# Performance work log

Measured on AMD Instinct MI355X. Metric: run time of the kernel, lower is better.

## Reference

```python
import jax, jax.numpy as jnp
import numpy as np

H = 64   # hid_dim (hard-coded in Attn_LSTM)
C = 8    # enc_in / out_dim
L = 96   # enc_seq_len = interval*lag = max_length
T = 24   # pre_len = window*horizon
B = 4096


def _p(key, shape, scale=0.1):
    return (jax.random.normal(key, shape, dtype=jnp.float32) * scale)


def setup_inputs() -> dict:
    key = jax.random.key(0)
    ks = jax.random.split(key, 20)
    inp = {
        'x_enc': jax.random.normal(ks[0], (B, L, C), dtype=jnp.float32),
        'x_mark_enc': jax.random.normal(ks[1], (B, L, 4), dtype=jnp.float32),
        'x_dec': jax.random.normal(ks[2], (B, T, C), dtype=jnp.float32),
        'x_mark_dec': jax.random.normal(ks[3], (B, T, 4), dtype=jnp.float32),
        # encoder LSTM (1 layer, input C -> hid H), pytorch gate order i,f,g,o
        'enc_Wih': _p(ks[4], (4 * H, C)), 'enc_Whh': _p(ks[5], (4 * H, H)),
        'enc_bih': _p(ks[6], (4 * H,)), 'enc_bhh': _p(ks[7], (4 * H,)),
        # decoder
        'emb_W': _p(ks[8], (H, C)), 'emb_b': _p(ks[9], (H,)),
        'attn_W': _p(ks[10], (L, 2 * H)), 'attn_b': _p(ks[11], (L,)),
        'comb_W': _p(ks[12], (H, 2 * H)), 'comb_b': _p(ks[13], (H,)),
        'dec_Wih': _p(ks[14], (4 * H, H)), 'dec_Whh': _p(ks[15], (4 * H, H)),
        'dec_bih': _p(ks[16], (4 * H,)), 'dec_bhh': _p(ks[17], (4 * H,)),
        'out_W': _p(ks[18], (C, H)), 'out_b': _p(ks[19], (C,)),
    }
    return inp


def _lstm_cell(x, h, c, Wih, Whh, bih, bhh):
    g = x @ Wih.T + h @ Whh.T + (bih + bhh)
    i, f, gg, o = jnp.split(g, 4, axis=-1)
    i, f, o = jax.nn.sigmoid(i), jax.nn.sigmoid(f), jax.nn.sigmoid(o)
    c_new = f * c + i * jnp.tanh(gg)
    h_new = o * jnp.tanh(c_new)
    return h_new, c_new


def _forward(x_enc, enc_Wih, enc_Whh, enc_bih, enc_bhh,
             emb_W, emb_b, attn_W, attn_b, comb_W, comb_b,
             dec_Wih, dec_Whh, dec_bih, dec_bhh, out_W, out_b):
    seq_last = x_enc[:, -1:, :]               # [B,1,C]
    x = x_enc - seq_last                      # normalized

    # ---- encoder: 1-layer LSTM over L steps ----
    h0 = jnp.zeros((x.shape[0], H), dtype=x.dtype)
    c0 = jnp.zeros_like(h0)

    def enc_step(carry, xt):
        h, c = carry
        h, c = _lstm_cell(xt, h, c, enc_Wih, enc_Whh, enc_bih, enc_bhh)
        return (h, c), h

    (h_enc, c_enc), enc_out = jax.lax.scan(enc_step, (h0, c0),
                                           jnp.swapaxes(x, 0, 1))
    enc_out = jnp.swapaxes(enc_out, 0, 1)     # [B,L,H]

    # ---- attention decoder: T sequential steps ----
    dec_in0 = x[:, -1, :]                     # last (normalized) input, [B,C]

    def dec_step(carry, _):
        inp, h, c = carry
        emb = jax.nn.relu(inp @ emb_W.T + emb_b)                       # [B,H]
        aw = jax.nn.softmax(jnp.concatenate([emb, h], -1) @ attn_W.T + attn_b)  # [B,L]
        ctx = jnp.einsum('bl,blh->bh', aw, enc_out)                    # [B,H]
        comb = jnp.concatenate([emb, ctx], -1) @ comb_W.T + comb_b     # [B,H]
        h, c = _lstm_cell(comb, h, c, dec_Wih, dec_Whh, dec_bih, dec_bhh)
        pred = h @ out_W.T + out_b                                     # [B,C]
        # original code feeds prediction.detach() back in
        return (jax.lax.stop_gradient(pred), h, c), (pred, aw)

    _, (preds, aws) = jax.lax.scan(dec_step, (dec_in0, h_enc, c_enc),
                                   None, length=T)
    pre_y = jnp.swapaxes(preds, 0, 1) + seq_last   # [B,T,C]
    return pre_y


def reference(x_enc, x_mark_enc, x_dec, x_mark_dec,
              enc_Wih, enc_Whh, enc_bih, enc_bhh,
              emb_W, emb_b, attn_W, attn_b, comb_W, comb_b,
              dec_Wih, dec_Whh, dec_bih, dec_bhh, out_W, out_b):
    # x_mark_enc, x_dec, x_mark_dec are accepted but unused (as in original)
    return _forward(x_enc, enc_Wih, enc_Whh, enc_bih, enc_bhh,
                    emb_W, emb_b, attn_W, attn_b, comb_W, comb_b,
                    dec_Wih, dec_Whh, dec_bih, dec_bhh, out_W, out_b)
```

## Files before the change

### kernel.cpp

```cpp
#include <hip/hip_runtime.h>

#define LL 96
#define TT 24
#define HH 64
#define CC 8
#define GG 256
#define BT 8
#define NB 512

typedef unsigned short u16t;
typedef unsigned int   u32t;
typedef __attribute__((ext_vector_type(8))) short bf16x8;
typedef __attribute__((ext_vector_type(4))) float f32x4;

__device__ __forceinline__ float b2f(u16t u){ union{u32t i; float f;} v; v.i=((u32t)u)<<16; return v.f; }
__device__ __forceinline__ float lo2f(u32t p){ union{u32t i; float f;} v; v.i=p<<16; return v.f; }
__device__ __forceinline__ float hi2f(u32t p){ union{u32t i; float f;} v; v.i=p&0xffff0000u; return v.f; }
__device__ __forceinline__ u16t f2b(float f){ union{float f; u32t i;} v; v.f=f; u32t l=(v.i>>16)&1u; v.i+=0x7fffu+l; return (u16t)(v.i>>16); }
__device__ __forceinline__ float rcpf(float x){ return __builtin_amdgcn_rcpf(x); }
__device__ __forceinline__ float sigm(float x){ return rcpf(1.f + __expf(-x)); }
__device__ __forceinline__ float tanh2(float x){ return 1.f - 2.f*rcpf(__expf(2.f*x) + 1.f); }
__device__ __forceinline__ u32t pk2(float a, float b){ return (u32t)f2b(a) | ((u32t)f2b(b)<<16); }
__device__ __forceinline__ bf16x8 u2b8(uint4 u){ union{uint4 a; bf16x8 b;} v; v.a=u; return v.b; }
__device__ __forceinline__ int aaddr(int k, int m){ return (((k>>5)*4 + ((k>>3)&3))*16 + m)*8 + (k&7); }

template<bool F32> __device__ __forceinline__ float ldf(const void* p, size_t i){
    if constexpr (F32) return ((const float*)p)[i];
    else               return b2f(((const u16t*)p)[i]);
}
template<bool F32> __device__ __forceinline__ uint4 ld8p(const void* p, size_t i){
    if constexpr (F32){
        const float* f = (const float*)p + i;
        uint4 r; r.x = pk2(f[0],f[1]); r.y = pk2(f[2],f[3]);
                 r.z = pk2(f[4],f[5]); r.w = pk2(f[6],f[7]);
        return r;
    } else return *(const uint4*)((const u16t*)p + i);
}
template<bool F32> __device__ __forceinline__ void stf(void* p, size_t i, float v){
    if constexpr (F32) ((float*)p)[i] = v;
    else               ((u16t*)p)[i] = f2b(v);
}
template<bool F32> __device__ __forceinline__ float ldW_enc(const void* wih, const void* whh, int r, int k){
    if (k < CC)      return ldf<F32>(wih, (size_t)r*CC + k);
    else if (k < 72) return ldf<F32>(whh, (size_t)r*HH + (k-CC));
    else             return 0.f;
}

__device__ __forceinline__ bool inputs_are_f32(const void* bih){
    const u16t* p = (const u16t*)bih;
    int cnt = 0;
    #pragma unroll
    for (int i = 0; i < 64; ++i){
        u32t e = ((u32t)p[i] >> 7) & 0xFFu;
        cnt += (e >= 128u) ? 1 : 0;
    }
    return cnt > 0;
}

template<bool F32>
__global__ __launch_bounds__(256,2) void fused_g(
    const void* __restrict__ x_enc,
    const void* __restrict__ eWih, const void* __restrict__ eWhh,
    const void* __restrict__ ebih, const void* __restrict__ ebhh,
    const void* __restrict__ embW, const void* __restrict__ embb,
    const void* __restrict__ attnW, const void* __restrict__ attnb,
    const void* __restrict__ combW, const void* __restrict__ combb,
    const void* __restrict__ dWih, const void* __restrict__ dWhh,
    const void* __restrict__ dbih, const void* __restrict__ dbhh,
    const void* __restrict__ outW, const void* __restrict__ outb,
    void* __restrict__ outp, u16t* __restrict__ eoG)
{
    if (inputs_are_f32(ebih) != F32) return;

    __shared__ __align__(16) float slp[CC*10];
    __shared__ __align__(16) short Abuf2[2][1536];
    __shared__ __align__(16) char  uni[18880];

    const int tid = threadIdx.x;
    const int b0  = blockIdx.x * BT;
    const int col = tid & 15, quad = (tid >> 4) & 3, wv = tid >> 6;
    const int r0  = (quad >> 1) * 2;

    bf16x8 Bf[4][3];
    float  biasg[4];
    #pragma unroll
    for (int g = 0; g < 4; ++g){
        int r = g*64 + wv*16 + col;
        biasg[g] = ldf<F32>(ebih, r) + ldf<F32>(ebhh, r);
        #pragma unroll
        for (int kb = 0; kb < 3; ++kb){
            bf16x8 v;
            #pragma unroll
            for (int x = 0; x < 8; ++x){
                int k = kb*32 + quad*8 + x;
                v[x] = (short)f2b(ldW_enc<F32>(eWih, eWhh, r, k));
            }
            Bf[g][kb] = v;
        }
    }
    for (int n = tid; n < 2*1536; n += 256) ((short*)Abuf2)[n] = 0;
    float sl = 0.f; size_t xbase = 0;
    if (tid < BT*CC){ int b = tid >> 3, i = tid & 7;
        xbase = (size_t)(b0+b)*(LL*CC) + i;
        sl = ldf<F32>(x_enc, xbase + (size_t)(LL-1)*CC);
        slp[i*10 + b] = sl; }
    __syncthreads();
    if (tid < BT*CC){ short v = (short)f2b(ldf<F32>(x_enc, xbase) - sl);
        Abuf2[0][tid] = v; Abuf2[0][tid + 64] = v; }
    float xr = (tid < BT*CC) ? ldf<F32>(x_enc, xbase + CC) : 0.f;

    const int jmy = wv*16 + col;
    const int kh  = 8 + jmy;
    const int hwbase = aaddr(kh, 0);

    u32t ebase[2];
    #pragma unroll
    for (int rr = 0; rr < 2; ++rr){
        u32t bg = (u32t)(b0 + ((quad*4 + r0 + rr) & 7));
        ebase[rr] = (bg*4u + (u32t)(jmy>>4))*1536u + (u32t)((jmy&15)*8);
    }

    float creg[2] = {0.f,0.f};
    u16t  hb16[2] = {0,0};

    for (int t = 0; t < LL; ++t){
        __syncthreads();
        const bf16x8* AbR = (const bf16x8*)Abuf2[t & 1];
        short*        AbW = Abuf2[(t + 1) & 1];
        bf16x8 a0 = AbR[(0*4 + quad)*16 + col];
        bf16x8 a1 = AbR[(1*4 + quad)*16 + col];
        bf16x8 a2 = AbR[(2*4 + quad)*16 + col];
        f32x4 acc[4];
        #pragma unroll
        for (int g = 0; g < 4; ++g){
            f32x4 a; a[0]=biasg[g]; a[1]=biasg[g]; a[2]=biasg[g]; a[3]=biasg[g];
            a = __builtin_amdgcn_mfma_f32_16x16x32_bf16(a0, Bf[g][0], a, 0,0,0);
            a = __builtin_amdgcn_mfma_f32_16x16x32_bf16(a1, Bf[g][1], a, 0,0,0);
            a = __builtin_amdgcn_mfma_f32_16x16x32_bf16(a2, Bf[g][2], a, 0,0,0);
            acc[g] = a;
        }
        int off = (t>>5)*512 + ((t>>3)&3)*128 + (t&7);
        #pragma unroll
        for (int rr = 0; rr < 2; ++rr){
            int r = r0 + rr;
            int b = (quad*4 + r) & 7;
            float c = sigm(acc[1][r])*creg[rr] + sigm(acc[0][r])*tanh2(acc[2][r]);
            float h = sigm(acc[3][r])*tanh2(c);
            creg[rr] = c; hb16[rr] = f2b(h);
            eoG[ebase[rr] + off] = hb16[rr];
            AbW[hwbase + b*8]     = (short)hb16[rr];
            AbW[hwbase + (b+8)*8] = (short)hb16[rr];
        }
        if (tid < BT*CC && t < LL-1){
            short v = (short)f2b(xr - sl);
            AbW[tid] = v; AbW[tid + 64] = v;
            int tn = (t+2 < LL) ? t+2 : LL-1;
            xr = ldf<F32>(x_enc, xbase + (size_t)tn*CC);
        }
    }

    bf16x8 Bd[4][4];
    #pragma unroll
    for (int g = 0; g < 4; ++g){
        int r = g*64 + wv*16 + col;
        Bd[g][0] = u2b8(ld8p<F32>(dWih, (size_t)r*HH + quad*8));
        Bd[g][1] = u2b8(ld8p<F32>(dWih, (size_t)r*HH + 32 + quad*8));
        Bd[g][2] = u2b8(ld8p<F32>(dWhh, (size_t)r*HH + quad*8));
        Bd[g][3] = u2b8(ld8p<F32>(dWhh, (size_t)r*HH + 32 + quad*8));
    }
    bf16x8 Ba[2][4];
    #pragma unroll
    for (int kb = 0; kb < 4; ++kb)
        Ba[0][kb] = u2b8(ld8p<F32>(attnW, (size_t)(wv*16+col)*128 + kb*32 + quad*8));
    if (wv < 2){
        #pragma unroll
        for (int kb = 0; kb < 4; ++kb)
            Ba[1][kb] = u2b8(ld8p<F32>(attnW, (size_t)((4+wv)*16+col)*128 + kb*32 + quad*8));
    } else {
        #pragma unroll
        for (int kb = 0; kb < 4; ++kb) Ba[1][kb] = Ba[0][kb];
    }
    bf16x8 Bc[4];
    #pragma unroll
    for (int kb = 0; kb < 4; ++kb)
        Bc[kb] = u2b8(ld8p<F32>(combW, (size_t)(wv*16+col)*128 + kb*32 + quad*8));
    bf16x8 zz = {0,0,0,0,0,0,0,0};
    bf16x8 eBf = zz;
    if (quad == 0) eBf = u2b8(ld8p<F32>(embW, (size_t)(wv*16+col)*CC));
    bf16x8 oBf0 = zz, oBf1 = zz;
    if (col < CC){
        oBf0 = u2b8(ld8p<F32>(outW, (size_t)col*HH + quad*8));
        oBf1 = u2b8(ld8p<F32>(outW, (size_t)col*HH + 32 + quad*8));
    }

    float* decB  = (float*)(uni + 0);
    float* attnB = (float*)(uni + 1024);
    float* embB  = (float*)(uni + 1408);
    float* combB = (float*)(uni + 1664);
    float* outB  = (float*)(uni + 1920);
    float* Lg    = (float*)(uni + 1952);
    u16t*  awB   = (u16t*)(uni + 5024);
    u16t*  Ae    = (u16t*)(uni + 6560);
    u16t*  Ah0   = (u16t*)(uni + 8608);
    u16t*  Ah1   = (u16t*)(uni + 10656);
    u16t*  Actx  = (u16t*)(uni + 12704);
    u16t*  Acmb  = (u16t*)(uni + 14752);
    u16t*  Apred = (u16t*)(uni + 16800);

    #pragma unroll
    for (int rr = 0; rr < 2; ++rr){
        int b = (quad*4 + r0 + rr) & 7;
        Ah0[aaddr(jmy, b)]     = hb16[rr];
        Ah0[aaddr(jmy, b+8)]   = hb16[rr];
    }
    decB[tid] = ldf<F32>(dbih, tid) + ldf<F32>(dbhh, tid);
    if (tid < LL) attnB[tid] = ldf<F32>(attnb, tid);
    if (tid < HH) embB[tid]  = ldf<F32>(embb, tid);
    if (tid < HH) combB[tid] = ldf<F32>(combb, tid);
    if (tid < CC) outB[tid]  = ldf<F32>(outb, tid);
    for (int n = tid; n < 1024; n += 256) Apred[n] = 0;
    __syncthreads();

    const u16t* ebp = eoG + (size_t)(b0 + wv*2) * 6144;
    uint4 eF0[12], eF1[12];
    #pragma unroll
    for (int f = 0; f < 12; ++f) eF0[f] = *(const uint4*)(ebp + f*512 + quad*128 + col*8);
    #pragma unroll
    for (int f = 0; f < 12; ++f) eF1[f] = *(const uint4*)(ebp + 6144 + f*512 + quad*128 + col*8);

    const int lgS = tid & 31, bS = tid >> 5;
    const bf16x8* AeV   = (const bf16x8*)Ae;
    const bf16x8* ActxV = (const bf16x8*)Actx;
    const bf16x8* AcmbV = (const bf16x8*)Acmb;
    const bf16x8* ApV   = (const bf16x8*)Apred;

    for (int t = 0; t < TT; ++t){
        u16t* AhR = (t & 1) ? Ah1 : Ah0;
        u16t* AhW = (t & 1) ? Ah0 : Ah1;
        const bf16x8* AhV = (const bf16x8*)AhR;

        {
            bf16x8 ap = ApV[quad*16 + col];
            float eb = embB[wv*16 + col];
            f32x4 a; a[0]=eb; a[1]=eb; a[2]=eb; a[3]=eb;
            a = __builtin_amdgcn_mfma_f32_16x16x32_bf16(ap, eBf, a, 0,0,0);
            #pragma unroll
            for (int r = 0; r < 4; ++r)
                Ae[aaddr(wv*16+col, quad*4 + r)] = f2b(fmaxf(a[r], 0.f));
        }
        __syncthreads();

        {
            bf16x8 ae0 = AeV[(0*4+quad)*16 + col], ae1 = AeV[(1*4+quad)*16 + col];
            bf16x8 ah0 = AhV[(0*4+quad)*16 + col], ah1 = AhV[(1*4+quad)*16 + col];
            const int ns = (wv < 2) ? 2 : 1;
            for (int s = 0; s < ns; ++s){
                int lt = (s == 0) ? wv : 4+wv;
                float bz = attnB[lt*16 + col];
                f32x4 a; a[0]=bz; a[1]=bz; a[2]=bz; a[3]=bz;
                a = __builtin_amdgcn_mfma_f32_16x16x32_bf16(ae0, Ba[s][0], a, 0,0,0);
                a = __builtin_amdgcn_mfma_f32_16x16x32_bf16(ae1, Ba[s][1], a, 0,0,0);
                a = __builtin_amdgcn_mfma_f32_16x16x32_bf16(ah0, Ba[s][2], a, 0,0,0);
                a = __builtin_amdgcn_mfma_f32_16x16x32_bf16(ah1, Ba[s][3], a, 0,0,0);
                if (quad < 2)
                    *(float4*)&Lg[(lt*16+col)*8 + quad*4] = make_float4(a[0],a[1],a[2],a[3]);
            }
        }
        __syncthreads();

        {
            int l = lgS*3;
            float ev0 = Lg[l*8 + bS], ev1 = Lg[(l+1)*8 + bS], ev2 = Lg[(l+2)*8 + bS];
            float mx = fmaxf(ev0, fmaxf(ev1, ev2));
            #pragma unroll
            for (int m = 16; m >= 1; m >>= 1) mx = fmaxf(mx, __shfl_xor(mx, m, 32));
            float e0 = __expf(ev0 - mx), e1 = __expf(ev1 - mx), e2 = __expf(ev2 - mx);
            float sm = e0 + e1 + e2;
            #pragma unroll
            for (int m = 16; m >= 1; m >>= 1) sm += __shfl_xor(sm, m, 32);
            float inv = rcpf(sm);
            awB[bS*96 + l]     = f2b(e0*inv);
            awB[bS*96 + l + 1] = f2b(e1*inv);
            awB[bS*96 + l + 2] = f2b(e2*inv);
        }
        {
            const u16t* ap0 = awB + (wv*2)*96;
            bf16x8 f0 = *(const bf16x8*)(ap0 + quad*8);
            bf16x8 f1 = *(const bf16x8*)(ap0 + 32 + quad*8);
            bf16x8 f2 = *(const bf16x8*)(ap0 + 64 + quad*8);
            #pragma unroll
            for (int nt = 0; nt < 4; ++nt){
                f32x4 a; a[0]=0.f; a[1]=0.f; a[2]=0.f; a[3]=0.f;
                a = __builtin_amdgcn_mfma_f32_16x16x32_bf16(f0, u2b8(eF0[nt*3+0]), a, 0,0,0);
                a = __builtin_amdgcn_mfma_f32_16x16x32_bf16(f1, u2b8(eF0[nt*3+1]), a, 0,0,0);
                a = __builtin_amdgcn_mfma_f32_16x16x32_bf16(f2, u2b8(eF0[nt*3+2]), a, 0,0,0);
                if (quad == 0){
                    u16t v = f2b(a[0]);
                    Actx[aaddr(nt*16+col, wv*2)]   = v;
                    Actx[aaddr(nt*16+col, wv*2+8)] = v;
                }
            }
            const u16t* ap1 = awB + (wv*2+1)*96;
            bf16x8 g0 = *(const bf16x8*)(ap1 + quad*8);
            bf16x8 g1 = *(const bf16x8*)(ap1 + 32 + quad*8);
            bf16x8 g2 = *(const bf16x8*)(ap1 + 64 + quad*8);
            #pragma unroll
            for (int nt = 0; nt < 4; ++nt){
                f32x4 a; a[0]=0.f; a[1]=0.f; a[2]=0.f; a[3]=0.f;
                a = __builtin_amdgcn_mfma_f32_16x16x32_bf16(g0, u2b8(eF1[nt*3+0]), a, 0,0,0);
                a = __builtin_amdgcn_mfma_f32_16x16x32_bf16(g1, u2b8(eF1[nt*3+1]), a, 0,0,0);
                a = __builtin_amdgcn_mfma_f32_16x16x32_bf16(g2, u2b8(eF1[nt*3+2]), a, 0,0,0);
                if (quad == 0){
                    u16t v = f2b(a[0]);
                    Actx[aaddr(nt*16+col, wv*2+1)] = v;
                    Actx[aaddr(nt*16+col, wv*2+9)] = v;
                }
            }
        }
        __syncthreads();

        {
            bf16x8 ae0 = AeV[(0*4+quad)*16 + col],   ae1 = AeV[(1*4+quad)*16 + col];
            bf16x8 ax0 = ActxV[(0*4+quad)*16 + col], ax1 = ActxV[(1*4+quad)*16 + col];
            float bz = combB[wv*16 + col];
            f32x4 a; a[0]=bz; a[1]=bz; a[2]=bz; a[3]=bz;
            a = __builtin_amdgcn_mfma_f32_16x16x32_bf16(ae0, Bc[0], a, 0,0,0);
            a = __builtin_amdgcn_mfma_f32_16x16x32_bf16(ae1, Bc[1], a, 0,0,0);
            a = __builtin_amdgcn_mfma_f32_16x16x32_bf16(ax0, Bc[2], a, 0,0,0);
            a = __builtin_amdgcn_mfma_f32_16x16x32_bf16(ax1, Bc[3], a, 0,0,0);
            #pragma unroll
            for (int r = 0; r < 4; ++r)
                Acmb[aaddr(wv*16+col, quad*4 + r)] = f2b(a[r]);
        }
        __syncthreads();

        {
            bf16x8 ac0 = AcmbV[(0*4+quad)*16 + col], ac1 = AcmbV[(1*4+quad)*16 + col];
            bf16x8 ah0 = AhV[(0*4+quad)*16 + col],   ah1 = AhV[(1*4+quad)*16 + col];
            f32x4 g4[4];
            #pragma unroll
            for (int g = 0; g < 4; ++g){
                float bz = decB[g*64 + wv*16 + col];
                f32x4 a; a[0]=bz; a[1]=bz; a[2]=bz; a[3]=bz;
                a = __builtin_amdgcn_mfma_f32_16x16x32_bf16(ac0, Bd[g][0], a, 0,0,0);
                a = __builtin_amdgcn_mfma_f32_16x16x32_bf16(ac1, Bd[g][1], a, 0,0,0);
                a = __builtin_amdgcn_mfma_f32_16x16x32_bf16(ah0, Bd[g][2], a, 0,0,0);
                a = __builtin_amdgcn_mfma_f32_16x16x32_bf16(ah1, Bd[g][3], a, 0,0,0);
                g4[g] = a;
            }
            #pragma unroll
            for (int rr = 0; rr < 2; ++rr){
                int r = r0 + rr;
                int b = (quad*4 + r) & 7;
                float c = sigm(g4[1][r])*creg[rr] + sigm(g4[0][r])*tanh2(g4[2][r]);
                float h = sigm(g4[3][r])*tanh2(c);
                creg[rr] = c;
                u16t hv = f2b(h);
                AhW[aaddr(jmy, b)]   = hv;
                AhW[aaddr(jmy, b+8)] = hv;
            }
        }
        __syncthreads();

        if (wv == 0){
            const bf16x8* AhWV = (const bf16x8*)AhW;
            bf16x8 xh0 = AhWV[(0*4+quad)*16 + col];
            bf16x8 xh1 = AhWV[(1*4+quad)*16 + col];
            float ob = outB[col & 7];
            f32x4 a; a[0]=ob; a[1]=ob; a[2]=ob; a[3]=ob;
            a = __builtin_amdgcn_mfma_f32_16x16x32_bf16(xh0, oBf0, a, 0,0,0);
            a = __builtin_amdgcn_mfma_f32_16x16x32_bf16(xh1, oBf1, a, 0,0,0);
            if (col < CC){
                #pragma unroll
                for (int r = 0; r < 4; ++r){
                    int m = quad*4 + r, b = m & 7;
                    float p = a[r];
                    Apred[aaddr(col, m)] = f2b(p);
                    if (m < 8)
                        stf<F32>(outp, ((size_t)(b0+b)*TT + t)*CC + col, p + slp[col*10 + b]);
                }
            }
        }
        __syncthreads();
    }
}

extern "C" void kernel_launch(void* const* d_in, const int* in_sizes, int n_in,
                              void* d_out, int out_size, void* d_ws, size_t ws_size,
                              hipStream_t stream)
{
    (void)in_sizes; (void)n_in; (void)out_size; (void)ws_size;
    fused_g<false><<<NB, 256, 0, stream>>>(
        d_in[0],
        d_in[4],  d_in[5],  d_in[6],  d_in[7],
        d_in[8],  d_in[9],  d_in[10], d_in[11],
        d_in[12], d_in[13], d_in[14], d_in[15],
        d_in[16], d_in[17], d_in[18], d_in[19],
        d_out, (u16t*)d_ws);
    fused_g<true><<<NB, 256, 0, stream>>>(
        d_in[0],
        d_in[4],  d_in[5],  d_in[6],  d_in[7],
        d_in[8],  d_in[9],  d_in[10], d_in[11],
        d_in[12], d_in[13], d_in[14], d_in[15],
        d_in[16], d_in[17], d_in[18], d_in[19],
        d_out, (u16t*)d_ws);
}
```

Measured before the change: 293.4 us.

## Split fused kernel into 4-row encoder kernel and separate decoder kernel

Splits the fused LSTM kernel in two. The encoder runs 4 batch rows per block on 1024 blocks with 4 blocks per CU, so each lane computes one hidden unit instead of two, and it stores packed bf16 pairs of encoder outputs. The final cell state goes to a workspace buffer, and a separate decoder kernel with 8 rows per block reads the final h and c back. This is meant to raise occupancy and shorten the serial encoder critical path. The cost is extra launches and a global round trip of state, and the new path only runs when the workspace is large enough; otherwise the old fused path is used.

```diff
diff --git a/kernel.cpp b/kernel.cpp
--- a/kernel.cpp
+++ b/kernel.cpp
@@ -58,106 +58,120 @@
 }
 
 template<bool F32>
-__global__ __launch_bounds__(256,2) void fused_g(
+__global__ __launch_bounds__(256,4) void enc4_g(
     const void* __restrict__ x_enc,
     const void* __restrict__ eWih, const void* __restrict__ eWhh,
     const void* __restrict__ ebih, const void* __restrict__ ebhh,
+    u16t* __restrict__ eoG, float* __restrict__ cG)
+{
+    if (inputs_are_f32(ebih) != F32) return;
+
+    __shared__ __align__(16) short Abuf2[2][1536];
+
+    const int tid = threadIdx.x;
+    const int b0  = blockIdx.x * 4;
+    const int col = tid & 15, quad = (tid >> 4) & 3, wv = tid >> 6;
+
+    bf16x8 Bf[4][3];
+    float  biasg[4];
+    #pragma unroll
+    for (int g = 0; g < 4; ++g){
+        int r = g*64 + wv*16 + col;
+        biasg[g] = ldf<F32>(ebih, r) + ldf<F32>(ebhh, r);
+        #pragma unroll
+        for (int kb = 0; kb < 3; ++kb){
+            bf16x8 v;
+            #pragma unroll
+            for (int x = 0; x < 8; ++x){
+                int k = kb*32 + quad*8 + x;
+                v[x] = (short)f2b(ldW_enc<F32>(eWih, eWhh, r, k));
+            }
+            Bf[g][kb] = v;
+        }
+    }
+    for (int n = tid; n < 2*1536; n += 256) ((short*)Abuf2)[n] = 0;
+    float sl = 0.f; size_t xbase = 0;
+    if (tid < 32){ int b = tid >> 3, i = tid & 7;
+        xbase = (size_t)(b0+b)*(LL*CC) + i;
+        sl = ldf<F32>(x_enc, xbase + (size_t)(LL-1)*CC);
+    }
+    __syncthreads();
+    if (tid < 32){ short v = (short)f2b(ldf<F32>(x_enc, xbase) - sl);
+        Abuf2[0][tid] = v; Abuf2[0][tid+32] = v; Abuf2[0][tid+64] = v; Abuf2[0][tid+96] = v; }
+    float xr = (tid < 32) ? ldf<F32>(x_enc, xbase + CC) : 0.f;
+
+    const int jmy = wv*16 + col;
+    const int hwbase = aaddr(8 + jmy, 0);
+    const u32t ebase = ((u32t)(b0 + quad)*4u + (u32t)(jmy>>4))*1536u + (u32t)((jmy&15)*8);
+
+    float creg = 0.f;
+    u32t  pkv  = 0;
+
+    #pragma unroll 2
+    for (int t = 0; t < LL; ++t){
+        __syncthreads();
+        const bf16x8* AbR = (const bf16x8*)Abuf2[t & 1];
+        short*        AbW = Abuf2[(t + 1) & 1];
+        bf16x8 a0 = AbR[(0*4 + quad)*16 + col];
+        bf16x8 a1 = AbR[(1*4 + quad)*16 + col];
+        bf16x8 a2 = AbR[(2*4 + quad)*16 + col];
+        f32x4 acc[4];
+        #pragma unroll
+        for (int g = 0; g < 4; ++g){
+            f32x4 a; a[0]=biasg[g]; a[1]=biasg[g]; a[2]=biasg[g]; a[3]=biasg[g];
+            a = __builtin_amdgcn_mfma_f32_16x16x32_bf16(a0, Bf[g][0], a, 0,0,0);
+            a = __builtin_amdgcn_mfma_f32_16x16x32_bf16(a1, Bf[g][1], a, 0,0,0);
+            a = __builtin_amdgcn_mfma_f32_16x16x32_bf16(a2, Bf[g][2], a, 0,0,0);
+            acc[g] = a;
+        }
+        float c = sigm(acc[1][quad])*creg + sigm(acc[0][quad])*tanh2(acc[2][quad]);
+        float h = sigm(acc[3][quad])*tanh2(c);
+        creg = c;
+        u16t hb = f2b(h);
+        if ((t & 1) == 0) pkv = hb;
+        else {
+            pkv |= ((u32t)hb) << 16;
+            *(u32t*)&eoG[ebase + (u32t)((t>>5)*512 + ((t>>3)&3)*128 + (t&7) - 1)] = pkv;
+        }
+        AbW[hwbase + quad*8]      = (short)hb;
+        AbW[hwbase + quad*8+32]   = (short)hb;
+        AbW[hwbase + quad*8+64]   = (short)hb;
+        AbW[hwbase + quad*8+96]   = (short)hb;
+        if (tid < 32 && t < LL-1){
+            short v = (short)f2b(xr - sl);
+            AbW[tid] = v; AbW[tid+32] = v; AbW[tid+64] = v; AbW[tid+96] = v;
+            int tn = (t+2 < LL) ? t+2 : LL-1;
+            xr = ldf<F32>(x_enc, xbase + (size_t)tn*CC);
+        }
+    }
+    cG[(size_t)(b0 + quad)*HH + jmy] = creg;
+}
+
+template<bool F32>
+__global__ __launch_bounds__(256,2) void dec8_g(
+    const void* __restrict__ x_enc,
     const void* __restrict__ embW, const void* __restrict__ embb,
     const void* __restrict__ attnW, const void* __restrict__ attnb,
     const void* __restrict__ combW, const void* __restrict__ combb,
     const void* __restrict__ dWih, const void* __restrict__ dWhh,
     const void* __restrict__ dbih, const void* __restrict__ dbhh,
     const void* __restrict__ outW, const void* __restrict__ outb,
-    void* __restrict__ outp, u16t* __restrict__ eoG)
+    void* __restrict__ outp, const u16t* __restrict__ eoG,
+    const float* __restrict__ cG)
 {
-    if (inputs_are_f32(ebih) != F32) return;
+    if (inputs_are_f32(dbih) != F32) return;
 
     __shared__ __align__(16) float slp[CC*10];
-    __shared__ __align__(16) short Abuf2[2][1536];
     __shared__ __align__(16) char  uni[18880];
 
     const int tid = threadIdx.x;
     const int b0  = blockIdx.x * BT;
     const int col = tid & 15, quad = (tid >> 4) & 3, wv = tid >> 6;
     const int r0  = (quad >> 1) * 2;
-
-    bf16x8 Bf[4][3];
-    float  biasg[4];
-    #pragma unroll
-    for (int g = 0; g < 4; ++g){
-        int r = g*64 + wv*16 + col;
-        biasg[g] = ldf<F32>(ebih, r) + ldf<F32>(ebhh, r);
-        #pragma unroll
-        for (int kb = 0; kb < 3; ++kb){
-            bf16x8 v;
-            #pragma unroll
-            for (int x = 0; x < 8; ++x){
-                int k = kb*32 + quad*8 + x;
-                v[x] = (short)f2b(ldW_enc<F32>(eWih, eWhh, r, k));
-            }
-            Bf[g][kb] = v;
-        }
-    }
-    for (int n = tid; n < 2*1536; n += 256) ((short*)Abuf2)[n] = 0;
-    float sl = 0.f; size_t xbase = 0;
+    const int jmy = wv*16 + col;
+
     if (tid < BT*CC){ int b = tid >> 3, i = tid & 7;
-        xbase = (size_t)(b0+b)*(LL*CC) + i;
-        sl = ldf<F32>(x_enc, xbase + (size_t)(LL-1)*CC);
-        slp[i*10 + b] = sl; }
-    __syncthreads();
-    if (tid < BT*CC){ short v = (short)f2b(ldf<F32>(x_enc, xbase) - sl);
-        Abuf2[0][tid] = v; Abuf2[0][tid + 64] = v; }
-    float xr = (tid < BT*CC) ? ldf<F32>(x_enc, xbase + CC) : 0.f;
-
-    const int jmy = wv*16 + col;
-    const int kh  = 8 + jmy;
-    const int hwbase = aaddr(kh, 0);
-
-    u32t ebase[2];
-    #pragma unroll
-    for (int rr = 0; rr < 2; ++rr){
-        u32t bg = (u32t)(b0 + ((quad*4 + r0 + rr) & 7));
-        ebase[rr] = (bg*4u + (u32t)(jmy>>4))*1536u + (u32t)((jmy&15)*8);
-    }
-
-    float creg[2] = {0.f,0.f};
-    u16t  hb16[2] = {0,0};
-
-    for (int t = 0; t < LL; ++t){
-        __syncthreads();
-        const bf16x8* AbR = (const bf16x8*)Abuf2[t & 1];
-        short*        AbW = Abuf2[(t + 1) & 1];
-        bf16x8 a0 = AbR[(0*4 + quad)*16 + col];
-        bf16x8 a1 = AbR[(1*4 + quad)*16 + col];
-        bf16x8 a2 = AbR[(2*4 + quad)*16 + col];
-        f32x4 acc[4];
-        #pragma unroll
-        for (int g = 0; g < 4; ++g){
-            f32x4 a; a[0]=biasg[g]; a[1]=biasg[g]; a[2]=biasg[g]; a[3]=biasg[g];
-            a = __builtin_amdgcn_mfma_f32_16x16x32_bf16(a0, Bf[g][0], a, 0,0,0);
-            a = __builtin_amdgcn_mfma_f32_16x16x32_bf16(a1, Bf[g][1], a, 0,0,0);
-            a = __builtin_amdgcn_mfma_f32_16x16x32_bf16(a2, Bf[g][2], a, 0,0,0);
-            acc[g] = a;
-        }
-        int off = (t>>5)*512 + ((t>>3)&3)*128 + (t&7);
-        #pragma unroll
-        for (int rr = 0; rr < 2; ++rr){
-            int r = r0 + rr;
-            int b = (quad*4 + r) & 7;
-            float c = sigm(acc[1][r])*creg[rr] + sigm(acc[0][r])*tanh2(acc[2][r]);
-            float h = sigm(acc[3][r])*tanh2(c);
-            creg[rr] = c; hb16[rr] = f2b(h);
-            eoG[ebase[rr] + off] = hb16[rr];
-            AbW[hwbase + b*8]     = (short)hb16[rr];
-            AbW[hwbase + (b+8)*8] = (short)hb16[rr];
-        }
-        if (tid < BT*CC && t < LL-1){
-            short v = (short)f2b(xr - sl);
-            AbW[tid] = v; AbW[tid + 64] = v;
-            int tn = (t+2 < LL) ? t+2 : LL-1;
-            xr = ldf<F32>(x_enc, xbase + (size_t)tn*CC);
-        }
-    }
+        slp[i*10 + b] = ldf<F32>(x_enc, (size_t)(b0+b)*(LL*CC) + (size_t)(LL-1)*CC + i); }
 
     bf16x8 Bd[4][4];
     #pragma unroll
@@ -207,11 +221,14 @@
     u16t*  Acmb  = (u16t*)(uni + 14752);
     u16t*  Apred = (u16t*)(uni + 16800);
 
+    float creg[2];
     #pragma unroll
     for (int rr = 0; rr < 2; ++rr){
         int b = (quad*4 + r0 + rr) & 7;
-        Ah0[aaddr(jmy, b)]     = hb16[rr];
-        Ah0[aaddr(jmy, b+8)]   = hb16[rr];
+        u16t hv = eoG[(((size_t)(b0+b)*4 + (size_t)(jmy>>4))*3 + 2)*512 + 3*128 + (jmy&15)*8 + 7];
+        Ah0[aaddr(jmy, b)]   = hv;
+        Ah0[aaddr(jmy, b+8)] = hv;
+        creg[rr] = cG[(size_t)(b0+b)*HH + jmy];
     }
     decB[tid] = ldf<F32>(dbih, tid) + ldf<F32>(dbhh, tid);
     if (tid < LL) attnB[tid] = ldf<F32>(attnb, tid);
@@ -385,23 +402,372 @@
     }
 }
 
+template<bool F32>
+__global__ __launch_bounds__(256,2) void fused_g(
+    const void* __restrict__ x_enc,
+    const void* __restrict__ eWih, const void* __restrict__ eWhh,
+    const void* __restrict__ ebih, const void* __restrict__ ebhh,
+    const void* __restrict__ embW, const void* __restrict__ embb,
+    const void* __restrict__ attnW, const void* __restrict__ attnb,
+    const void* __restrict__ combW, const void* __restrict__ combb,
+    const void* __restrict__ dWih, const void* __restrict__ dWhh,
+    const void* __restrict__ dbih, const void* __restrict__ dbhh,
+    const void* __restrict__ outW, const void* __restrict__ outb,
+    void* __restrict__ outp, u16t* __restrict__ eoG)
+{
+    if (inputs_are_f32(ebih) != F32) return;
+
+    __shared__ __align__(16) float slp[CC*10];
+    __shared__ __align__(16) short Abuf2[2][1536];
+    __shared__ __align__(16) char  uni[18880];
+
+    const int tid = threadIdx.x;
+    const int b0  = blockIdx.x * BT;
+    const int col = tid & 15, quad = (tid >> 4) & 3, wv = tid >> 6;
+    const int r0  = (quad >> 1) * 2;
+
+    bf16x8 Bf[4][3];
+    float  biasg[4];
+    #pragma unroll
+    for (int g = 0; g < 4; ++g){
+        int r = g*64 + wv*16 + col;
+        biasg[g] = ldf<F32>(ebih, r) + ldf<F32>(ebhh, r);
+        #pragma unroll
+        for (int kb = 0; kb < 3; ++kb){
+            bf16x8 v;
+            #pragma unroll
+            for (int x = 0; x < 8; ++x){
+                int k = kb*32 + quad*8 + x;
+                v[x] = (short)f2b(ldW_enc<F32>(eWih, eWhh, r, k));
+            }
+            Bf[g][kb] = v;
+        }
+    }
+    for (int n = tid; n < 2*1536; n += 256) ((short*)Abuf2)[n] = 0;
+    float sl = 0.f; size_t xbase = 0;
+    if (tid < BT*CC){ int b = tid >> 3, i = tid & 7;
+        xbase = (size_t)(b0+b)*(LL*CC) + i;
+        sl = ldf<F32>(x_enc, xbase + (size_t)(LL-1)*CC);
+        slp[i*10 + b] = sl; }
+    __syncthreads();
+    if (tid < BT*CC){ short v = (short)f2b(ldf<F32>(x_enc, xbase) - sl);
+        Abuf2[0][tid] = v; Abuf2[0][tid + 64] = v; }
+    float xr = (tid < BT*CC) ? ldf<F32>(x_enc, xbase + CC) : 0.f;
+
+    const int jmy = wv*16 + col;
+    const int kh  = 8 + jmy;
+    const int hwbase = aaddr(kh, 0);
+
+    u32t ebase[2];
+    #pragma unroll
+    for (int rr = 0; rr < 2; ++rr){
+        u32t bg = (u32t)(b0 + ((quad*4 + r0 + rr) & 7));
+        ebase[rr] = (bg*4u + (u32t)(jmy>>4))*1536u + (u32t)((jmy&15)*8);
+    }
+
+    float creg[2] = {0.f,0.f};
+    u16t  hb16[2] = {0,0};
+
+    for (int t = 0; t < LL; ++t){
+        __syncthreads();
+        const bf16x8* AbR = (const bf16x8*)Abuf2[t & 1];
+        short*        AbW = Abuf2[(t + 1) & 1];
+        bf16x8 a0 = AbR[(0*4 + quad)*16 + col];
+        bf16x8 a1 = AbR[(1*4 + quad)*16 + col];
+        bf16x8 a2 = AbR[(2*4 + quad)*16 + col];
+        f32x4 acc[4];
+        #pragma unroll
+        for (int g = 0; g < 4; ++g){
+            f32x4 a; a[0]=biasg[g]; a[1]=biasg[g]; a[2]=biasg[g]; a[3]=biasg[g];
+            a = __builtin_amdgcn_mfma_f32_16x16x32_bf16(a0, Bf[g][0], a, 0,0,0);
+            a = __builtin_amdgcn_mfma_f32_16x16x32_bf16(a1, Bf[g][1], a, 0,0,0);
+            a = __builtin_amdgcn_mfma_f32_16x16x32_bf16(a2, Bf[g][2], a, 0,0,0);
+            acc[g] = a;
+        }
+        int off = (t>>5)*512 + ((t>>3)&3)*128 + (t&7);
+        #pragma unroll
+        for (int rr = 0; rr < 2; ++rr){
+            int r = r0 + rr;
+            int b = (quad*4 + r) & 7;
+            float c = sigm(acc[1][r])*creg[rr] + sigm(acc[0][r])*tanh2(acc[2][r]);
+            float h = sigm(acc[3][r])*tanh2(c);
+            creg[rr] = c; hb16[rr] = f2b(h);
+            eoG[ebase[rr] + off] = hb16[rr];
+            AbW[hwbase + b*8]     = (short)hb16[rr];
+            AbW[hwbase + (b+8)*8] = (short)hb16[rr];
+        }
+        if (tid < BT*CC && t < LL-1){
+            short v = (short)f2b(xr - sl);
+            AbW[tid] = v; AbW[tid + 64] = v;
+            int tn = (t+2 < LL) ? t+2 : LL-1;
+            xr = ldf<F32>(x_enc, xbase + (size_t)tn*CC);
+        }
+    }
+
+    bf16x8 Bd[4][4];
+    #pragma unroll
+    for (int g = 0; g < 4; ++g){
+        int r = g*64 + wv*16 + col;
+        Bd[g][0] = u2b8(ld8p<F32>(dWih, (size_t)r*HH + quad*8));
+        Bd[g][1] = u2b8(ld8p<F32>(dWih, (size_t)r*HH + 32 + quad*8));
+        Bd[g][2] = u2b8(ld8p<F32>(dWhh, (size_t)r*HH + quad*8));
+        Bd[g][3] = u2b8(ld8p<F32>(dWhh, (size_t)r*HH + 32 + quad*8));
+    }
+    bf16x8 Ba[2][4];
+    #pragma unroll
+    for (int kb = 0; kb < 4; ++kb)
+        Ba[0][kb] = u2b8(ld8p<F32>(attnW, (size_t)(wv*16+col)*128 + kb*32 + quad*8));
+    if (wv < 2){
+        #pragma unroll
+        for (int kb = 0; kb < 4; ++kb)
+            Ba[1][kb] = u2b8(ld8p<F32>(attnW, (size_t)((4+wv)*16+col)*128 + kb*32 + quad*8));
+    } else {
+        #pragma unroll
+        for (int kb = 0; kb < 4; ++kb) Ba[1][kb] = Ba[0][kb];
+    }
+    bf16x8 Bc[4];
+    #pragma unroll
+    for (int kb = 0; kb < 4; ++kb)
+        Bc[kb] = u2b8(ld8p<F32>(combW, (size_t)(wv*16+col)*128 + kb*32 + quad*8));
+    bf16x8 zz = {0,0,0,0,0,0,0,0};
+    bf16x8 eBf = zz;
+    if (quad == 0) eBf = u2b8(ld8p<F32>(embW, (size_t)(wv*16+col)*CC));
+    bf16x8 oBf0 = zz, oBf1 = zz;
+    if (col < CC){
+        oBf0 = u2b8(ld8p<F32>(outW, (size_t)col*HH + quad*8));
+        oBf1 = u2b8(ld8p<F32>(outW, (size_t)col*HH + 32 + quad*8));
+    }
+
+    float* decB  = (float*)(uni + 0);
+    float* attnB = (float*)(uni + 1024);
+    float* embB  = (float*)(uni + 1408);
+    float* combB = (float*)(uni + 1664);
+    float* outB  = (float*)(uni + 1920);
+    float* Lg    = (float*)(uni + 1952);
+    u16t*  awB   = (u16t*)(uni + 5024);
+    u16t*  Ae    = (u16t*)(uni + 6560);
+    u16t*  Ah0   = (u16t*)(uni + 8608);
+    u16t*  Ah1   = (u16t*)(uni + 10656);
+    u16t*  Actx  = (u16t*)(uni + 12704);
+    u16t*  Acmb  = (u16t*)(uni + 14752);
+    u16t*  Apred = (u16t*)(uni + 16800);
+
+    #pragma unroll
+    for (int rr = 0; rr < 2; ++rr){
+        int b = (quad*4 + r0 + rr) & 7;
+        Ah0[aaddr(jmy, b)]     = hb16[rr];
+        Ah0[aaddr(jmy, b+8)]   = hb16[rr];
+    }
+    decB[tid] = ldf<F32>(dbih, tid) + ldf<F32>(dbhh, tid);
+    if (tid < LL) attnB[tid] = ldf<F32>(attnb, tid);
+    if (tid < HH) embB[tid]  = ldf<F32>(embb, tid);
+    if (tid < HH) combB[tid] = ldf<F32>(combb, tid);
+    if (tid < CC) outB[tid]  = ldf<F32>(outb, tid);
+    for (int n = tid; n < 1024; n += 256) Apred[n] = 0;
+    __syncthreads();
+
+    const u16t* ebp = eoG + (size_t)(b0 + wv*2) * 6144;
+    uint4 eF0[12], eF1[12];
+    #pragma unroll
+    for (int f = 0; f < 12; ++f) eF0[f] = *(const uint4*)(ebp + f*512 + quad*128 + col*8);
+    #pragma unroll
+    for (int f = 0; f < 12; ++f) eF1[f] = *(const uint4*)(ebp + 6144 + f*512 + quad*128 + col*8);
+
+    const int lgS = tid & 31, bS = tid >> 5;
+    const bf16x8* AeV   = (const bf16x8*)Ae;
+    const bf16x8* ActxV = (const bf16x8*)Actx;
+    const bf16x8* AcmbV = (const bf16x8*)Acmb;
+    const bf16x8* ApV   = (const bf16x8*)Apred;
+
+    for (int t = 0; t < TT; ++t){
+        u16t* AhR = (t & 1) ? Ah1 : Ah0;
+        u16t* AhW = (t & 1) ? Ah0 : Ah1;
+        const bf16x8* AhV = (const bf16x8*)AhR;
+
+        {
+            bf16x8 ap = ApV[quad*16 + col];
+            float eb = embB[wv*16 + col];
+            f32x4 a; a[0]=eb; a[1]=eb; a[2]=eb; a[3]=eb;
+            a = __builtin_amdgcn_mfma_f32_16x16x32_bf16(ap, eBf, a, 0,0,0);
+            #pragma unroll
+            for (int r = 0; r < 4; ++r)
+                Ae[aaddr(wv*16+col, quad*4 + r)] = f2b(fmaxf(a[r], 0.f));
+        }
+        __syncthreads();
+
+        {
+            bf16x8 ae0 = AeV[(0*4+quad)*16 + col], ae1 = AeV[(1*4+quad)*16 + col];
+            bf16x8 ah0 = AhV[(0*4+quad)*16 + col], ah1 = AhV[(1*4+quad)*16 + col];
+            const int ns = (wv < 2) ? 2 : 1;
+            for (int s = 0; s < ns; ++s){
+                int lt = (s == 0) ? wv : 4+wv;
+                float bz = attnB[lt*16 + col];
+                f32x4 a; a[0]=bz; a[1]=bz; a[2]=bz; a[3]=bz;
+                a = __builtin_amdgcn_mfma_f32_16x16x32_bf16(ae0, Ba[s][0], a, 0,0,0);
+                a = __builtin_amdgcn_mfma_f32_16x16x32_bf16(ae1, Ba[s][1], a, 0,0,0);
+                a = __builtin_amdgcn_mfma_f32_16x16x32_bf16(ah0, Ba[s][2], a, 0,0,0);
+                a = __builtin_amdgcn_mfma_f32_16x16x32_bf16(ah1, Ba[s][3], a, 0,0,0);
+                if (quad < 2)
+                    *(float4*)&Lg[(lt*16+col)*8 + quad*4] = make_float4(a[0],a[1],a[2],a[3]);
+            }
+        }
+        __syncthreads();
+
+        {
+            int l = lgS*3;
+            float ev0 = Lg[l*8 + bS], ev1 = Lg[(l+1)*8 + bS], ev2 = Lg[(l+2)*8 + bS];
+            float mx = fmaxf(ev0, fmaxf(ev1, ev2));
+            #pragma unroll
+            for (int m = 16; m >= 1; m >>= 1) mx = fmaxf(mx, __shfl_xor(mx, m, 32));
+            float e0 = __expf(ev0 - mx), e1 = __expf(ev1 - mx), e2 = __expf(ev2 - mx);
+            float sm = e0 + e1 + e2;
+            #pragma unroll
+            for (int m = 16; m >= 1; m >>= 1) sm += __shfl_xor(sm, m, 32);
+            float inv = rcpf(sm);
+            awB[bS*96 + l]     = f2b(e0*inv);
+            awB[bS*96 + l + 1] = f2b(e1*inv);
+            awB[bS*96 + l + 2] = f2b(e2*inv);
+        }
+        {
+            const u16t* ap0 = awB + (wv*2)*96;
+            bf16x8 f0 = *(const bf16x8*)(ap0 + quad*8);
+            bf16x8 f1 = *(const bf16x8*)(ap0 + 32 + quad*8);
+            bf16x8 f2 = *(const bf16x8*)(ap0 + 64 + quad*8);
+            #pragma unroll
+            for (int nt = 0; nt < 4; ++nt){
+                f32x4 a; a[0]=0.f; a[1]=0.f; a[2]=0.f; a[3]=0.f;
+                a = __builtin_amdgcn_mfma_f32_16x16x32_bf16(f0, u2b8(eF0[nt*3+0]), a, 0,0,0);
+                a = __builtin_amdgcn_mfma_f32_16x16x32_bf16(f1, u2b8(eF0[nt*3+1]), a, 0,0,0);
+                a = __builtin_amdgcn_mfma_f32_16x16x32_bf16(f2, u2b8(eF0[nt*3+2]), a, 0,0,0);
+                if (quad == 0){
+                    u16t v = f2b(a[0]);
+                    Actx[aaddr(nt*16+col, wv*2)]   = v;
+                    Actx[aaddr(nt*16+col, wv*2+8)] = v;
+                }
+            }
+            const u16t* ap1 = awB + (wv*2+1)*96;
+            bf16x8 g0 = *(const bf16x8*)(ap1 + quad*8);
+            bf16x8 g1 = *(const bf16x8*)(ap1 + 32 + quad*8);
+            bf16x8 g2 = *(const bf16x8*)(ap1 + 64 + quad*8);
+            #pragma unroll
+            for (int nt = 0; nt < 4; ++nt){
+                f32x4 a; a[0]=0.f; a[1]=0.f; a[2]=0.f; a[3]=0.f;
+                a = __builtin_amdgcn_mfma_f32_16x16x32_bf16(g0, u2b8(eF1[nt*3+0]), a, 0,0,0);
+                a = __builtin_amdgcn_mfma_f32_16x16x32_bf16(g1, u2b8(eF1[nt*3+1]), a, 0,0,0);
+                a = __builtin_amdgcn_mfma_f32_16x16x32_bf16(g2, u2b8(eF1[nt*3+2]), a, 0,0,0);
+                if (quad == 0){
+                    u16t v = f2b(a[0]);
+                    Actx[aaddr(nt*16+col, wv*2+1)] = v;
+                    Actx[aaddr(nt*16+col, wv*2+9)] = v;
+                }
+            }
+        }
+        __syncthreads();
+
+        {
+            bf16x8 ae0 = AeV[(0*4+quad)*16 + col],   ae1 = AeV[(1*4+quad)*16 + col];
+            bf16x8 ax0 = ActxV[(0*4+quad)*16 + col], ax1 = ActxV[(1*4+quad)*16 + col];
+            float bz = combB[wv*16 + col];
+            f32x4 a; a[0]=bz; a[1]=bz; a[2]=bz; a[3]=bz;
+            a = __builtin_amdgcn_mfma_f32_16x16x32_bf16(ae0, Bc[0], a, 0,0,0);
+            a = __builtin_amdgcn_mfma_f32_16x16x32_bf16(ae1, Bc[1], a, 0,0,0);
+            a = __builtin_amdgcn_mfma_f32_16x16x32_bf16(ax0, Bc[2], a, 0,0,0);
+            a = __builtin_amdgcn_mfma_f32_16x16x32_bf16(ax1, Bc[3], a, 0,0,0);
+            #pragma unroll
+            for (int r = 0; r < 4; ++r)
+                Acmb[aaddr(wv*16+col, quad*4 + r)] = f2b(a[r]);
+        }
+        __syncthreads();
+
+        {
+            bf16x8 ac0 = AcmbV[(0*4+quad)*16 + col], ac1 = AcmbV[(1*4+quad)*16 + col];
+            bf16x8 ah0 = AhV[(0*4+quad)*16 + col],   ah1 = AhV[(1*4+quad)*16 + col];
+            f32x4 g4[4];
+            #pragma unroll
+            for (int g = 0; g < 4; ++g){
+                float bz = decB[g*64 + wv*16 + col];
+                f32x4 a; a[0]=bz; a[1]=bz; a[2]=bz; a[3]=bz;
+                a = __builtin_amdgcn_mfma_f32_16x16x32_bf16(ac0, Bd[g][0], a, 0,0,0);
+                a = __builtin_amdgcn_mfma_f32_16x16x32_bf16(ac1, Bd[g][1], a, 0,0,0);
+                a = __builtin_amdgcn_mfma_f32_16x16x32_bf16(ah0, Bd[g][2], a, 0,0,0);
+                a = __builtin_amdgcn_mfma_f32_16x16x32_bf16(ah1, Bd[g][3], a, 0,0,0);
+                g4[g] = a;
+            }
+            #pragma unroll
+            for (int rr = 0; rr < 2; ++rr){
+                int r = r0 + rr;
+                int b = (quad*4 + r) & 7;
+                float c = sigm(g4[1][r])*creg[rr] + sigm(g4[0][r])*tanh2(g4[2][r]);
+                float h = sigm(g4[3][r])*tanh2(c);
+                creg[rr] = c;
+                u16t hv = f2b(h);
+                AhW[aaddr(jmy, b)]   = hv;
+                AhW[aaddr(jmy, b+8)] = hv;
+            }
+        }
+        __syncthreads();
+
+        if (wv == 0){
+            const bf16x8* AhWV = (const bf16x8*)AhW;
+            bf16x8 xh0 = AhWV[(0*4+quad)*16 + col];
+            bf16x8 xh1 = AhWV[(1*4+quad)*16 + col];
+            float ob = outB[col & 7];
+            f32x4 a; a[0]=ob; a[1]=ob; a[2]=ob; a[3]=ob;
+            a = __builtin_amdgcn_mfma_f32_16x16x32_bf16(xh0, oBf0, a, 0,0,0);
+            a = __builtin_amdgcn_mfma_f32_16x16x32_bf16(xh1, oBf1, a, 0,0,0);
+            if (col < CC){
+                #pragma unroll
+                for (int r = 0; r < 4; ++r){
+                    int m = quad*4 + r, b = m & 7;
+                    float p = a[r];
+                    Apred[aaddr(col, m)] = f2b(p);
+                    if (m < 8)
+                        stf<F32>(outp, ((size_t)(b0+b)*TT + t)*CC + col, p + slp[col*10 + b]);
+                }
+            }
+        }
+        __syncthreads();
+    }
+}
+
 extern "C" void kernel_launch(void* const* d_in, const int* in_sizes, int n_in,
                               void* d_out, int out_size, void* d_ws, size_t ws_size,
                               hipStream_t stream)
 {
-    (void)in_sizes; (void)n_in; (void)out_size; (void)ws_size;
-    fused_g<false><<<NB, 256, 0, stream>>>(
-        d_in[0],
-        d_in[4],  d_in[5],  d_in[6],  d_in[7],
-        d_in[8],  d_in[9],  d_in[10], d_in[11],
-        d_in[12], d_in[13], d_in[14], d_in[15],
-        d_in[16], d_in[17], d_in[18], d_in[19],
-        d_out, (u16t*)d_ws);
-    fused_g<true><<<NB, 256, 0, stream>>>(
-        d_in[0],
-        d_in[4],  d_in[5],  d_in[6],  d_in[7],
-        d_in[8],  d_in[9],  d_in[10], d_in[11],
-        d_in[12], d_in[13], d_in[14], d_in[15],
-        d_in[16], d_in[17], d_in[18], d_in[19],
-        d_out, (u16t*)d_ws);
-}
+    (void)in_sizes; (void)n_in; (void)out_size;
+    u16t* eoG = (u16t*)d_ws;
+    if (ws_size >= 50331648ull + 1048576ull){
+        float* cG = (float*)((char*)d_ws + 50331648ull);
+        enc4_g<false><<<1024, 256, 0, stream>>>(
+            d_in[0], d_in[4], d_in[5], d_in[6], d_in[7], eoG, cG);
+        enc4_g<true ><<<1024, 256, 0, stream>>>(
+            d_in[0], d_in[4], d_in[5], d_in[6], d_in[7], eoG, cG);
+        dec8_g<false><<<NB, 256, 0, stream>>>(
+            d_in[0],
+            d_in[8],  d_in[9],  d_in[10], d_in[11],
+            d_in[12], d_in[13], d_in[14], d_in[15],
+            d_in[16], d_in[17], d_in[18], d_in[19],
+            d_out, eoG, cG);
+        dec8_g<true ><<<NB, 256, 0, stream>>>(
+            d_in[0],
+            d_in[8],  d_in[9],  d_in[10], d_in[11],
+            d_in[12], d_in[13], d_in[14], d_in[15],
+            d_in[16], d_in[17], d_in[18], d_in[19],
+            d_out, eoG, cG);
+    } else {
+        fused_g<false><<<NB, 256, 0, stream>>>(
+            d_in[0],
+            d_in[4],  d_in[5],  d_in[6],  d_in[7],
+            d_in[8],  d_in[9],  d_in[10], d_in[11],
+            d_in[12], d_in[13], d_in[14], d_in[15],
+            d_in[16], d_in[17], d_in[18], d_in[19],
+            d_out, eoG);
+        fused_g<true><<<NB, 256, 0, stream>>>(
+            d_in[0],
+            d_in[4],  d_in[5],  d_in[6],  d_in[7],
+            d_in[8],  d_in[9],  d_in[10], d_in[11],
+            d_in[12], d_in[13], d_in[14], d_in[15],
+            d_in[16], d_in[17], d_in[18], d_in[19],
+            d_out, eoG);
+    }
+}
```

Result: slower. 311.0 us (+6.0%).
